# Kernel tuning notes

Hardware: AMD Instinct MI355X
Metric: run time of the kernel (lower is better)

The kernel has to match this reference:

```python
import jax, jax.numpy as jnp
import numpy as np
import math

N, IN_DIM, Z, H, OUT, K = 16384, 64, 128, 1, 3, 16


def setup_inputs() -> dict:
    key = jax.random.key(0)
    ks = jax.random.split(key, 16)

    def lin(k, din, dout):
        kw, kb = jax.random.split(k)
        W = jax.random.normal(kw, (din, dout), jnp.float32) / math.sqrt(din)
        b = jax.random.normal(kb, (dout,), jnp.float32) * 0.01
        return W, b

    x = jax.random.normal(ks[0], (N, IN_DIM), jnp.float32)
    t = jnp.zeros((1,), jnp.float32)
    # layer dims: (in, heads*out) per TransformerConv
    dims = [(IN_DIM, Z * H), (Z * H, (Z // H) * H), (Z * H, (OUT // H) * H)]
    params = {}
    i = 1
    for li, (din, dout) in enumerate(dims, 1):
        for nm in ("q", "k", "v", "s"):
            W, b = lin(ks[i], din, dout)
            i += 1
            params[f"W{nm}{li}"] = W
            params[f"b{nm}{li}"] = b
    return {"t": t, "x": x, **params}


def knn_edge_index(coo, k):
    # kNN graph on 3-D coords (loop=False): edges neighbor(src) -> center(dst)
    n = coo.shape[0]
    sq = jnp.sum(coo * coo, axis=-1)
    d = sq[:, None] + sq[None, :] - 2.0 * (coo @ coo.T)  # [N, N] sq. distances
    d = d.at[jnp.arange(n), jnp.arange(n)].set(jnp.inf)  # exclude self-loops
    _, idx = jax.lax.top_k(-d, k)  # [N, K] nearest neighbor indices
    src = idx.reshape(-1)
    dst = jnp.repeat(jnp.arange(n), k)
    return src, dst


def tconv(x, src, dst, Wq, bq, Wk, bk, Wv, bv, Ws, bs, heads):
    # PyG TransformerConv (concat=True, root_weight=True, no edge_attr)
    n = x.shape[0]
    dout = Wq.shape[1]
    c = dout // heads
    q = (x @ Wq + bq).reshape(n, heads, c)
    kk = (x @ Wk + bk).reshape(n, heads, c)
    v = (x @ Wv + bv).reshape(n, heads, c)
    alpha = jnp.sum(q[dst] * kk[src], axis=-1) / math.sqrt(c)  # [E, H]
    amax = jax.ops.segment_max(alpha, dst, num_segments=n)
    ex = jnp.exp(alpha - amax[dst])
    denom = jax.ops.segment_sum(ex, dst, num_segments=n)
    w = ex / denom[dst]  # softmax over incoming edges per node
    msg = w[:, :, None] * v[src]  # [E, H, C]
    out = jax.ops.segment_sum(msg, dst, num_segments=n).reshape(n, dout)
    return out + x @ Ws + bs  # root/skip connection


def reference(t, x,
              Wq1, bq1, Wk1, bk1, Wv1, bv1, Ws1, bs1,
              Wq2, bq2, Wk2, bk2, Wv2, bv2, Ws2, bs2,
              Wq3, bq3, Wk3, bk3, Wv3, bv3, Ws3, bs3):
    src, dst = knn_edge_index(x[:, :3], K)  # built under no_grad in original
    h = jnp.tanh(tconv(x, src, dst, Wq1, bq1, Wk1, bk1, Wv1, bv1, Ws1, bs1, H))
    h = jnp.tanh(tconv(h, src, dst, Wq2, bq2, Wk2, bk2, Wv2, bv2, Ws2, bs2, H) + h)
    drift_coo = tconv(h, src, dst, Wq3, bq3, Wk3, bk3, Wv3, bv3, Ws3, bs3, H)
    return drift_coo
```

## Files before the change

kernel.cpp:

```cpp
#include <hip/hip_runtime.h>
#include <math.h>

#define NN 16384
#define QPW 2
#define CAP 128
#define WM 64
#define KTOP 17

typedef unsigned long long u64;

__global__ __launch_bounds__(256) void pack_coords(const float* __restrict__ x,
                                                   float4* __restrict__ coo) {
  int i = blockIdx.x * 256 + threadIdx.x;
  float a = x[i * 64 + 0];
  float b = x[i * 64 + 1];
  float c = x[i * 64 + 2];
  coo[i] = make_float4(a, b, c, a * a + b * b + c * c);
}

__device__ __forceinline__ int mbcnt64(u64 mask) {
  return __builtin_amdgcn_mbcnt_hi(
      (unsigned)(mask >> 32),
      __builtin_amdgcn_mbcnt_lo((unsigned)mask, 0));
}

__device__ __forceinline__ unsigned fmap(float d) {
  unsigned ub = __float_as_uint(d);
  return ub ^ ((unsigned)((int)ub >> 31) | 0x80000000u);
}

__device__ __forceinline__ float unfmap(unsigned ub) {
  unsigned fb = (ub & 0x80000000u) ? (ub ^ 0x80000000u) : ~ub;
  return __uint_as_float(fb);
}

__device__ __forceinline__ unsigned short f2bf(float f) {
  unsigned u = __float_as_uint(f);
  return (unsigned short)((u + 0x7FFFu + ((u >> 16) & 1u)) >> 16);
}
__device__ __forceinline__ float bf2f(unsigned short h) {
  return __uint_as_float(((unsigned)h) << 16);
}

__device__ __forceinline__ u64 u64min(u64 a, u64 b) { return a < b ? a : b; }
__device__ __forceinline__ u64 u64max(u64 a, u64 b) { return a > b ? a : b; }

__device__ __forceinline__ void sort128(u64& r0, u64& r1, int lane) {
#pragma unroll
  for (int k = 2; k <= 128; k <<= 1) {
    if (k == 128) {
      u64 lo = u64min(r0, r1);
      r1 = u64max(r0, r1);
      r0 = lo;
    }
#pragma unroll
    for (int jj = (k == 128 ? 32 : (k >> 1)); jj >= 1; jj >>= 1) {
      const bool up = (lane & jj) == 0;
      const bool asc0 = (lane & k) == 0;
      const bool asc1 = ((lane | 64) & k) == 0;
      u64 o0 = __shfl_xor(r0, jj);
      u64 o1 = __shfl_xor(r1, jj);
      r0 = (up == asc0) ? u64min(r0, o0) : u64max(r0, o0);
      r1 = (up == asc1) ? u64min(r1, o1) : u64max(r1, o1);
    }
  }
}

__device__ __forceinline__ void radix_shrink(u64* buf, int& cnt, float& th,
                                             int lane) {
  const u64 k0 = (lane < cnt) ? buf[lane] : ~0ull;
  const u64 k1 = (lane + 64 < cnt) ? buf[lane + 64] : ~0ull;
  const unsigned d0 = (unsigned)(k0 >> 32);
  const unsigned d1 = (unsigned)(k1 >> 32);
  unsigned p = 0u;
#pragma unroll
  for (int b = 31; b >= 0; --b) {
    const unsigned c = p | (1u << b);
    const u64 b0 = __ballot(d0 < c);
    const u64 b1 = __ballot(d1 < c);
    const int n = __popcll(b0) + __popcll(b1);
    if (n < KTOP) p = c;
  }
  const bool v0 = d0 <= p;
  const bool v1 = d1 <= p;
  const u64 m0 = __ballot(v0);
  const u64 m1 = __ballot(v1);
  const int base = __popcll(m0);
  if (v0) buf[mbcnt64(m0)] = k0;
  if (v1) buf[base + mbcnt64(m1)] = k1;
  cnt = base + __popcll(m1);
  th = unfmap(p);
}

__global__ __launch_bounds__(256) void knn_kernel(const float4* __restrict__ coo,
                                                  int* __restrict__ src) {
  __shared__ u64 bufs[4][QPW][CAP];
  const int lane = threadIdx.x & 63;
  const int wid = threadIdx.x >> 6;
  const int node0 = blockIdx.x * (4 * QPW) + wid * QPW;

  float nx[QPW], ny[QPW], nz[QPW], sq[QPW], th[QPW];
  int cnt[QPW];
#pragma unroll
  for (int q = 0; q < QPW; ++q) {
    const float4 me = coo[node0 + q];
    nx[q] = -2.0f * me.x;
    ny[q] = -2.0f * me.y;
    nz[q] = -2.0f * me.z;
    sq[q] = me.w;
    cnt[q] = 0;
  }

  {
    const float4 pa = coo[lane];
    const float4 pb = coo[64 + lane];
#pragma unroll
    for (int q = 0; q < QPW; ++q) {
      const float d0 = sq[q] + fmaf(nx[q], pa.x,
                           fmaf(ny[q], pa.y, fmaf(nz[q], pa.z, pa.w)));
      const float d1 = sq[q] + fmaf(nx[q], pb.x,
                           fmaf(ny[q], pb.y, fmaf(nz[q], pb.z, pb.w)));
      bufs[wid][q][lane] = ((u64)fmap(d0) << 32) | (unsigned)lane;
      bufs[wid][q][64 + lane] = ((u64)fmap(d1) << 32) | (unsigned)(64 + lane);
      cnt[q] = 128;
      radix_shrink(bufs[wid][q], cnt[q], th[q], lane);
    }
  }

  float4 s0 = coo[2 * 64 + lane];
  float4 s1 = coo[3 * 64 + lane];
  float4 s2 = coo[4 * 64 + lane];
  float4 s3 = coo[5 * 64 + lane];

  auto body = [&](const float4 cur, const int step) {
    const int j = step * 64 + lane;
    float dd[QPW];
#pragma unroll
    for (int q = 0; q < QPW; ++q)
      dd[q] = sq[q] + fmaf(nx[q], cur.x,
                           fmaf(ny[q], cur.y, fmaf(nz[q], cur.z, cur.w)));
    u64 mk[QPW];
#pragma unroll
    for (int q = 0; q < QPW; ++q) mk[q] = __ballot(dd[q] <= th[q]);
    if (mk[0] | mk[1]) {
#pragma unroll
      for (int q = 0; q < QPW; ++q) {
        if (mk[q]) {
          if (dd[q] <= th[q])
            bufs[wid][q][cnt[q] + mbcnt64(mk[q])] =
                ((u64)fmap(dd[q]) << 32) | (unsigned)j;
          cnt[q] += __popcll(mk[q]);
          if (cnt[q] >= WM) radix_shrink(bufs[wid][q], cnt[q], th[q], lane);
        }
      }
    }
  };

#pragma unroll 1
  for (int g = 0; g < 63; ++g) {
    const int base = 2 + g * 4;
    body(s0, base + 0);
    s0 = coo[(base + 4) * 64 + lane];
    body(s1, base + 1);
    s1 = coo[(base + 5) * 64 + lane];
    body(s2, base + 2);
    s2 = coo[(base + 6) * 64 + lane];
    body(s3, base + 3);
    s3 = coo[(base + 7) * 64 + lane];
  }
  body(s0, 254);
  body(s1, 255);

#pragma unroll 1
  for (int q = 0; q < QPW; ++q) {
    u64 r0 = (lane < cnt[q]) ? bufs[wid][q][lane] : ~0ull;
    u64 r1 = (lane + 64 < cnt[q]) ? bufs[wid][q][lane + 64] : ~0ull;
    sort128(r0, r1, lane);
    const int idx = (int)(r0 & 0xFFFFFFFFull);
    const u64 selfm = __ballot((lane < KTOP) && (idx == node0 + q));
    const int s = selfm ? (__ffsll((long long)selfm) - 1) : 99;
    const int outrank = lane - (lane > s ? 1 : 0);
    if (lane < KTOP && lane != s && outrank < 16)
      src[(node0 + q) * 16 + outrank] = idx;
  }
}

template <int KD>
__global__ __launch_bounds__(256) void gemm_qkvs(
    const float* __restrict__ X, const float* __restrict__ W0,
    const float* __restrict__ W1, const float* __restrict__ W2,
    const float* __restrict__ W3, const float* __restrict__ B0,
    const float* __restrict__ B1, const float* __restrict__ B2,
    const float* __restrict__ B3, float* __restrict__ qs,
    unsigned short* __restrict__ kvh) {
  __shared__ float As[64][68];
  __shared__ float Bs[64][64];
  const int brow = blockIdx.x * 64;
  const int by = blockIdx.y;
  const int wi = by >> 1;
  const float* W = wi == 0 ? W0 : wi == 1 ? W1 : wi == 2 ? W2 : W3;
  const float* bias = wi == 0 ? B0 : wi == 1 ? B1 : wi == 2 ? B2 : B3;
  const int cbase = (by & 1) * 64;
  const int tx = threadIdx.x & 15;
  const int ty = threadIdx.x >> 4;

  float acc[4][4] = {};
  for (int k0 = 0; k0 < KD; k0 += 64) {
    __syncthreads();
#pragma unroll
    for (int i = 0; i < 4; ++i) {
      const int flat = threadIdx.x * 4 + i * 1024;
      const int r = flat >> 6, kk = flat & 63;
      const float4 v = *(const float4*)&X[(brow + r) * KD + k0 + kk];
      As[kk + 0][r] = v.x;
      As[kk + 1][r] = v.y;
      As[kk + 2][r] = v.z;
      As[kk + 3][r] = v.w;
    }
#pragma unroll
    for (int i = 0; i < 4; ++i) {
      const int flat = threadIdx.x * 4 + i * 1024;
      const int kk = flat >> 6, c = flat & 63;
      *(float4*)&Bs[kk][c] = *(const float4*)&W[(k0 + kk) * 128 + cbase + c];
    }
    __syncthreads();
#pragma unroll 8
    for (int k = 0; k < 64; ++k) {
      const float4 a = *(const float4*)&As[k][ty * 4];
      const float4 b = *(const float4*)&Bs[k][tx * 4];
      const float av[4] = {a.x, a.y, a.z, a.w};
      const float bv[4] = {b.x, b.y, b.z, b.w};
#pragma unroll
      for (int i = 0; i < 4; ++i)
#pragma unroll
        for (int jj = 0; jj < 4; ++jj)
          acc[i][jj] = fmaf(av[i], bv[jj], acc[i][jj]);
    }
  }
  const float4 bi = *(const float4*)&bias[cbase + tx * 4];
  const int col = cbase + tx * 4;
#pragma unroll
  for (int i = 0; i < 4; ++i) {
    const int row = brow + ty * 4 + i;
    float4 o;
    o.x = acc[i][0] + bi.x;
    o.y = acc[i][1] + bi.y;
    o.z = acc[i][2] + bi.z;
    o.w = acc[i][3] + bi.w;
    if (wi == 0) {
      *(float4*)&qs[row * 256 + col] = o;
    } else if (wi == 3) {
      *(float4*)&qs[row * 256 + 128 + col] = o;
    } else {
      ushort4 h;
      h.x = f2bf(o.x);
      h.y = f2bf(o.y);
      h.z = f2bf(o.z);
      h.w = f2bf(o.w);
      *(ushort4*)&kvh[row * 256 + (wi == 1 ? col : 128 + col)] = h;
    }
  }
}

__global__ __launch_bounds__(256) void attn_c128(
    const float* __restrict__ qs, const unsigned short* __restrict__ kvh,
    const int* __restrict__ src, const float* __restrict__ res,
    float* __restrict__ hout, int do_res) {
  const int g = threadIdx.x >> 5;
  const int node = blockIdx.x * 8 + g;
  const int c = threadIdx.x & 31;
  const float4 q4 = ((const float4*)(qs + node * 256))[c];

  int nb[16];
#pragma unroll
  for (int r = 0; r < 16; ++r) nb[r] = src[node * 16 + r];

  float p[16];
#pragma unroll
  for (int r = 0; r < 16; ++r) {
    const ushort4 k4 = ((const ushort4*)(kvh + nb[r] * 256))[c];
    p[r] = q4.x * bf2f(k4.x) + q4.y * bf2f(k4.y) + q4.z * bf2f(k4.z) +
           q4.w * bf2f(k4.w);
  }
#pragma unroll
  for (int o = 16; o; o >>= 1) {
#pragma unroll
    for (int r = 0; r < 16; ++r) p[r] += __shfl_xor(p[r], o);
  }

  float m = p[0];
#pragma unroll
  for (int r = 1; r < 16; ++r) m = fmaxf(m, p[r]);
  float w[16];
  float den = 0.0f;
#pragma unroll
  for (int r = 0; r < 16; ++r) {
    w[r] = __expf((p[r] - m) * 0.088388347648318447f);
    den += w[r];
  }
  const float inv = 1.0f / den;
  float o0 = 0.0f, o1 = 0.0f, o2 = 0.0f, o3 = 0.0f;
#pragma unroll
  for (int r = 0; r < 16; ++r) {
    const ushort4 v4 = ((const ushort4*)(kvh + nb[r] * 256 + 128))[c];
    const float ww = w[r] * inv;
    o0 = fmaf(ww, bf2f(v4.x), o0);
    o1 = fmaf(ww, bf2f(v4.y), o1);
    o2 = fmaf(ww, bf2f(v4.z), o2);
    o3 = fmaf(ww, bf2f(v4.w), o3);
  }
  const float4 s4 = ((const float4*)(qs + node * 256 + 128))[c];
  float r0 = o0 + s4.x, r1 = o1 + s4.y, r2 = o2 + s4.z, r3 = o3 + s4.w;
  if (do_res) {
    const float4 h4 = ((const float4*)(res + node * 128))[c];
    r0 += h4.x;
    r1 += h4.y;
    r2 += h4.z;
    r3 += h4.w;
  }
  ((float4*)(hout + node * 128))[c] =
      make_float4(tanhf(r0), tanhf(r1), tanhf(r2), tanhf(r3));
}

__global__ __launch_bounds__(256) void gemm_qkvs3(
    const float* __restrict__ H, const float* __restrict__ W0,
    const float* __restrict__ W1, const float* __restrict__ W2,
    const float* __restrict__ W3, const float* __restrict__ B0,
    const float* __restrict__ B1, const float* __restrict__ B2,
    const float* __restrict__ B3, float* __restrict__ out) {
  __shared__ float hs[64][132];
  __shared__ float wsh[128 * 12];
  __shared__ float bsh[12];
  const int brow = blockIdx.x * 64;
  if (threadIdx.x < 12) {
    const int mi = threadIdx.x / 3, c = threadIdx.x % 3;
    const float* Bsel = mi == 0 ? B0 : mi == 1 ? B1 : mi == 2 ? B2 : B3;
    bsh[threadIdx.x] = Bsel[c];
  }
  for (int t = threadIdx.x; t < 1536; t += 256) {
    const int k = t / 12, cc = t % 12;
    const int mi = cc / 3, c = cc % 3;
    const float* Wsel = mi == 0 ? W0 : mi == 1 ? W1 : mi == 2 ? W2 : W3;
    wsh[t] = Wsel[k * 3 + c];
  }
#pragma unroll
  for (int i = 0; i < 8; ++i) {
    const int flat = threadIdx.x * 4 + i * 1024;
    const int r = flat >> 7, kk = flat & 127;
    *(float4*)&hs[r][kk] = *(const float4*)&H[(brow + r) * 128 + kk];
  }
  __syncthreads();
  const int r = threadIdx.x >> 2;
  const int part = threadIdx.x & 3;
  float a0 = 0.0f, a1 = 0.0f, a2 = 0.0f;
#pragma unroll 4
  for (int k = 0; k < 128; ++k) {
    const float h = hs[r][k];
    a0 = fmaf(h, wsh[k * 12 + part * 3 + 0], a0);
    a1 = fmaf(h, wsh[k * 12 + part * 3 + 1], a1);
    a2 = fmaf(h, wsh[k * 12 + part * 3 + 2], a2);
  }
  const int row = brow + r;
  out[row * 12 + part * 3 + 0] = a0 + bsh[part * 3 + 0];
  out[row * 12 + part * 3 + 1] = a1 + bsh[part * 3 + 1];
  out[row * 12 + part * 3 + 2] = a2 + bsh[part * 3 + 2];
}

__global__ __launch_bounds__(256) void attn_c3(const float* __restrict__ q3,
                                               const int* __restrict__ src,
                                               float* __restrict__ out) {
  const int gid = blockIdx.x * 256 + threadIdx.x;
  const int node = gid >> 4, r = gid & 15;
  const int j = src[node * 16 + r];
  const float* qn = q3 + node * 12;
  const float* kj = q3 + j * 12 + 3;
  float alpha = (qn[0] * kj[0] + qn[1] * kj[1] + qn[2] * kj[2]) *
                0.57735026918962576f;
  float m = alpha;
#pragma unroll
  for (int o = 8; o; o >>= 1) m = fmaxf(m, __shfl_xor(m, o, 16));
  const float e = __expf(alpha - m);
  float den = e;
#pragma unroll
  for (int o = 8; o; o >>= 1) den += __shfl_xor(den, o, 16);
  const float wgt = e / den;
  const float* vj = q3 + j * 12 + 6;
  float o0 = wgt * vj[0], o1 = wgt * vj[1], o2 = wgt * vj[2];
#pragma unroll
  for (int o = 8; o; o >>= 1) {
    o0 += __shfl_xor(o0, o, 16);
    o1 += __shfl_xor(o1, o, 16);
    o2 += __shfl_xor(o2, o, 16);
  }
  if (r == 0) {
    const float* sn = q3 + node * 12 + 9;
    out[node * 3 + 0] = o0 + sn[0];
    out[node * 3 + 1] = o1 + sn[1];
    out[node * 3 + 2] = o2 + sn[2];
  }
}

extern "C" void kernel_launch(void* const* d_in, const int* in_sizes, int n_in,
                              void* d_out, int out_size, void* d_ws,
                              size_t ws_size, hipStream_t stream) {
  const float* x = (const float*)d_in[1];
  const float* Wq1 = (const float*)d_in[2];
  const float* bq1 = (const float*)d_in[3];
  const float* Wk1 = (const float*)d_in[4];
  const float* bk1 = (const float*)d_in[5];
  const float* Wv1 = (const float*)d_in[6];
  const float* bv1 = (const float*)d_in[7];
  const float* Ws1 = (const float*)d_in[8];
  const float* bs1 = (const float*)d_in[9];
  const float* Wq2 = (const float*)d_in[10];
  const float* bq2 = (const float*)d_in[11];
  const float* Wk2 = (const float*)d_in[12];
  const float* bk2 = (const float*)d_in[13];
  const float* Wv2 = (const float*)d_in[14];
  const float* bv2 = (const float*)d_in[15];
  const float* Ws2 = (const float*)d_in[16];
  const float* bs2 = (const float*)d_in[17];
  const float* Wq3 = (const float*)d_in[18];
  const float* bq3 = (const float*)d_in[19];
  const float* Wk3 = (const float*)d_in[20];
  const float* bk3 = (const float*)d_in[21];
  const float* Wv3 = (const float*)d_in[22];
  const float* bv3 = (const float*)d_in[23];
  const float* Ws3 = (const float*)d_in[24];
  const float* bs3 = (const float*)d_in[25];

  const size_t MB = 1024 * 1024;
  char* ws = (char*)d_ws;
  float* qs = (float*)(ws);
  unsigned short* kvh = (unsigned short*)(ws + 16 * MB);
  float* h1 = (float*)(ws + 24 * MB);
  float* h2 = (float*)(ws + 32 * MB);
  int* src = (int*)(ws + 40 * MB);
  float4* coo = (float4*)(ws + 41 * MB);
  float* q3 = (float*)(ws + 42 * MB);
  float* out = (float*)d_out;

  pack_coords<<<NN / 256, 256, 0, stream>>>(x, coo);
  knn_kernel<<<NN / (4 * QPW), 256, 0, stream>>>(coo, src);
  gemm_qkvs<64><<<dim3(NN / 64, 8), 256, 0, stream>>>(
      x, Wq1, Wk1, Wv1, Ws1, bq1, bk1, bv1, bs1, qs, kvh);
  attn_c128<<<NN / 8, 256, 0, stream>>>(qs, kvh, src, nullptr, h1, 0);
  gemm_qkvs<128><<<dim3(NN / 64, 8), 256, 0, stream>>>(
      h1, Wq2, Wk2, Wv2, Ws2, bq2, bk2, bv2, bs2, qs, kvh);
  attn_c128<<<NN / 8, 256, 0, stream>>>(qs, kvh, src, h1, h2, 1);
  gemm_qkvs3<<<NN / 64, 256, 0, stream>>>(h2, Wq3, Wk3, Wv3, Ws3, bq3, bk3,
                                          bv3, bs3, q3);
  attn_c3<<<NN * 16 / 256, 256, 0, stream>>>(q3, src, out);
}
```

Before: 306.1 us.

## Replace brute-force kNN with uniform-grid spatial search

Replaces the O(N^2) brute-force kNN scan with a uniform 32^3 grid. A count/scan/scatter pass bins points into cells, then each wavefront searches outward shell by shell and stops once the current 17th-best distance is within the distance to the shell boundary. This removes the full scan over all 16384 candidates per query that dominated the runtime, at the cost of several small extra launches and atomics. Within-cell scatter order is set by atomics, so the order of candidates with equal distances can differ from before.

```diff
diff --git a/kernel.cpp b/kernel.cpp
--- a/kernel.cpp
+++ b/kernel.cpp
@@ -6,6 +6,10 @@
 #define CAP 128
 #define WM 64
 #define KTOP 17
+#define G 32
+#define GLO (-6.0f)
+#define GW (12.0f / G)
+#define GINVW (G / 12.0f)
 
 typedef unsigned long long u64;
 
@@ -92,97 +96,152 @@
   th = unfmap(p);
 }
 
-__global__ __launch_bounds__(256) void knn_kernel(const float4* __restrict__ coo,
-                                                  int* __restrict__ src) {
-  __shared__ u64 bufs[4][QPW][CAP];
+__device__ __forceinline__ int cell_of(float v) {
+  int c = (int)floorf((v - GLO) * GINVW);
+  return min(max(c, 0), G - 1);
+}
+
+__global__ __launch_bounds__(256) void grid_zero(int* __restrict__ counts) {
+  counts[blockIdx.x * 256 + threadIdx.x] = 0;
+}
+
+__global__ __launch_bounds__(256) void grid_count(const float4* __restrict__ coo,
+                                                  int* __restrict__ counts) {
+  const int i = blockIdx.x * 256 + threadIdx.x;
+  const float4 p = coo[i];
+  const int cell = (cell_of(p.z) * G + cell_of(p.y)) * G + cell_of(p.x);
+  atomicAdd(&counts[cell], 1);
+}
+
+__global__ __launch_bounds__(1024) void grid_scan(const int* __restrict__ counts,
+                                                  int* __restrict__ cellStart,
+                                                  int* __restrict__ cursor) {
+  __shared__ int part[1024];
+  const int t = threadIdx.x;
+  const int base = t * (G * G * G / 1024);
+  int sum = 0;
+  for (int i = 0; i < G * G * G / 1024; ++i) sum += counts[base + i];
+  part[t] = sum;
+  __syncthreads();
+  for (int off = 1; off < 1024; off <<= 1) {
+    int v = (t >= off) ? part[t - off] : 0;
+    __syncthreads();
+    part[t] += v;
+    __syncthreads();
+  }
+  int run = (t == 0) ? 0 : part[t - 1];
+  for (int i = 0; i < G * G * G / 1024; ++i) {
+    const int c = counts[base + i];
+    cellStart[base + i] = run;
+    cursor[base + i] = run;
+    run += c;
+  }
+  if (t == 1023) cellStart[G * G * G] = run;
+}
+
+__global__ __launch_bounds__(256) void grid_scatter(
+    const float4* __restrict__ coo, int* __restrict__ cursor,
+    float4* __restrict__ scoo, int* __restrict__ sidx) {
+  const int i = blockIdx.x * 256 + threadIdx.x;
+  const float4 p = coo[i];
+  const int cell = (cell_of(p.z) * G + cell_of(p.y)) * G + cell_of(p.x);
+  const int pos = atomicAdd(&cursor[cell], 1);
+  scoo[pos] = p;
+  sidx[pos] = i;
+}
+
+__global__ __launch_bounds__(256) void knn_grid(
+    const float4* __restrict__ scoo, const int* __restrict__ sidx,
+    const int* __restrict__ cellStart, const float4* __restrict__ coo,
+    int* __restrict__ src) {
+  __shared__ u64 bufs[4][CAP];
   const int lane = threadIdx.x & 63;
   const int wid = threadIdx.x >> 6;
-  const int node0 = blockIdx.x * (4 * QPW) + wid * QPW;
-
-  float nx[QPW], ny[QPW], nz[QPW], sq[QPW], th[QPW];
-  int cnt[QPW];
-#pragma unroll
-  for (int q = 0; q < QPW; ++q) {
-    const float4 me = coo[node0 + q];
-    nx[q] = -2.0f * me.x;
-    ny[q] = -2.0f * me.y;
-    nz[q] = -2.0f * me.z;
-    sq[q] = me.w;
-    cnt[q] = 0;
-  }
-
-  {
-    const float4 pa = coo[lane];
-    const float4 pb = coo[64 + lane];
-#pragma unroll
-    for (int q = 0; q < QPW; ++q) {
-      const float d0 = sq[q] + fmaf(nx[q], pa.x,
-                           fmaf(ny[q], pa.y, fmaf(nz[q], pa.z, pa.w)));
-      const float d1 = sq[q] + fmaf(nx[q], pb.x,
-                           fmaf(ny[q], pb.y, fmaf(nz[q], pb.z, pb.w)));
-      bufs[wid][q][lane] = ((u64)fmap(d0) << 32) | (unsigned)lane;
-      bufs[wid][q][64 + lane] = ((u64)fmap(d1) << 32) | (unsigned)(64 + lane);
-      cnt[q] = 128;
-      radix_shrink(bufs[wid][q], cnt[q], th[q], lane);
-    }
-  }
-
-  float4 s0 = coo[2 * 64 + lane];
-  float4 s1 = coo[3 * 64 + lane];
-  float4 s2 = coo[4 * 64 + lane];
-  float4 s3 = coo[5 * 64 + lane];
-
-  auto body = [&](const float4 cur, const int step) {
-    const int j = step * 64 + lane;
-    float dd[QPW];
-#pragma unroll
-    for (int q = 0; q < QPW; ++q)
-      dd[q] = sq[q] + fmaf(nx[q], cur.x,
-                           fmaf(ny[q], cur.y, fmaf(nz[q], cur.z, cur.w)));
-    u64 mk[QPW];
-#pragma unroll
-    for (int q = 0; q < QPW; ++q) mk[q] = __ballot(dd[q] <= th[q]);
-    if (mk[0] | mk[1]) {
-#pragma unroll
-      for (int q = 0; q < QPW; ++q) {
-        if (mk[q]) {
-          if (dd[q] <= th[q])
-            bufs[wid][q][cnt[q] + mbcnt64(mk[q])] =
-                ((u64)fmap(dd[q]) << 32) | (unsigned)j;
-          cnt[q] += __popcll(mk[q]);
-          if (cnt[q] >= WM) radix_shrink(bufs[wid][q], cnt[q], th[q], lane);
+  const int node = blockIdx.x * 4 + wid;
+  u64* buf = bufs[wid];
+
+  const float4 me = coo[node];
+  const float nx = -2.0f * me.x, ny = -2.0f * me.y, nz = -2.0f * me.z;
+  const float sq = me.w;
+  const int hx = cell_of(me.x), hy = cell_of(me.y), hz = cell_of(me.z);
+
+  float th = __builtin_inff();
+  int cnt = 0;
+
+  auto runrange = [&](int x0, int x1, int y, int z) {
+    const int b = (z * G + y) * G;
+    const int rs = cellStart[b + x0];
+    const int re = cellStart[b + x1 + 1];
+    for (int bs = rs; bs < re; bs += 64) {
+      const int i = bs + lane;
+      const int ic = min(i, NN - 1);
+      const float4 p = scoo[ic];
+      const int id = sidx[ic];
+      float acc = fmaf(nz, p.z, p.w);
+      acc = fmaf(ny, p.y, acc);
+      acc = fmaf(nx, p.x, acc);
+      const float d = sq + acc;
+      const bool val = (i < re) && (d <= th);
+      const u64 mk = __ballot(val);
+      if (mk) {
+        if (val)
+          buf[cnt + mbcnt64(mk)] = ((u64)fmap(d) << 32) | (unsigned)id;
+        cnt += __popcll(mk);
+        if (cnt >= WM) radix_shrink(buf, cnt, th, lane);
+      }
+    }
+  };
+
+  for (int dz = -1; dz <= 1; ++dz) {
+    const int z = hz + dz;
+    if (z < 0 || z >= G) continue;
+    for (int dy = -1; dy <= 1; ++dy) {
+      const int y = hy + dy;
+      if (y < 0 || y >= G) continue;
+      runrange(max(hx - 1, 0), min(hx + 1, G - 1), y, z);
+    }
+  }
+
+  int s = 1;
+  while (true) {
+    if (cnt >= KTOP) {
+      radix_shrink(buf, cnt, th, lane);
+      float dmin = 1e30f;
+      if (hx - s > 0) dmin = fminf(dmin, me.x - (GLO + (hx - s) * GW));
+      if (hx + s < G - 1) dmin = fminf(dmin, (GLO + (hx + s + 1) * GW) - me.x);
+      if (hy - s > 0) dmin = fminf(dmin, me.y - (GLO + (hy - s) * GW));
+      if (hy + s < G - 1) dmin = fminf(dmin, (GLO + (hy + s + 1) * GW) - me.y);
+      if (hz - s > 0) dmin = fminf(dmin, me.z - (GLO + (hz - s) * GW));
+      if (hz + s < G - 1) dmin = fminf(dmin, (GLO + (hz + s + 1) * GW) - me.z);
+      dmin = fmaxf(dmin, 0.0f);
+      if (th <= dmin * dmin * 0.9999f) break;
+    }
+    ++s;
+    if (s > G) break;
+    for (int dz = -s; dz <= s; ++dz) {
+      const int z = hz + dz;
+      if (z < 0 || z >= G) continue;
+      for (int dy = -s; dy <= s; ++dy) {
+        const int y = hy + dy;
+        if (y < 0 || y >= G) continue;
+        if (dz == -s || dz == s || dy == -s || dy == s) {
+          runrange(max(hx - s, 0), min(hx + s, G - 1), y, z);
+        } else {
+          if (hx - s >= 0) runrange(hx - s, hx - s, y, z);
+          if (hx + s <= G - 1) runrange(hx + s, hx + s, y, z);
         }
       }
     }
-  };
-
-#pragma unroll 1
-  for (int g = 0; g < 63; ++g) {
-    const int base = 2 + g * 4;
-    body(s0, base + 0);
-    s0 = coo[(base + 4) * 64 + lane];
-    body(s1, base + 1);
-    s1 = coo[(base + 5) * 64 + lane];
-    body(s2, base + 2);
-    s2 = coo[(base + 6) * 64 + lane];
-    body(s3, base + 3);
-    s3 = coo[(base + 7) * 64 + lane];
-  }
-  body(s0, 254);
-  body(s1, 255);
-
-#pragma unroll 1
-  for (int q = 0; q < QPW; ++q) {
-    u64 r0 = (lane < cnt[q]) ? bufs[wid][q][lane] : ~0ull;
-    u64 r1 = (lane + 64 < cnt[q]) ? bufs[wid][q][lane + 64] : ~0ull;
-    sort128(r0, r1, lane);
-    const int idx = (int)(r0 & 0xFFFFFFFFull);
-    const u64 selfm = __ballot((lane < KTOP) && (idx == node0 + q));
-    const int s = selfm ? (__ffsll((long long)selfm) - 1) : 99;
-    const int outrank = lane - (lane > s ? 1 : 0);
-    if (lane < KTOP && lane != s && outrank < 16)
-      src[(node0 + q) * 16 + outrank] = idx;
-  }
+  }
+
+  u64 r0 = (lane < cnt) ? buf[lane] : ~0ull;
+  u64 r1 = (lane + 64 < cnt) ? buf[lane + 64] : ~0ull;
+  sort128(r0, r1, lane);
+  const int idx = (int)(r0 & 0xFFFFFFFFull);
+  const u64 selfm = __ballot((lane < KTOP) && (idx == node));
+  const int sf = selfm ? (__ffsll((long long)selfm) - 1) : 99;
+  const int outrank = lane - (lane > sf ? 1 : 0);
+  if (lane < KTOP && lane != sf && outrank < 16) src[node * 16 + outrank] = idx;
 }
 
 template <int KD>
@@ -438,10 +497,19 @@
   int* src = (int*)(ws + 40 * MB);
   float4* coo = (float4*)(ws + 41 * MB);
   float* q3 = (float*)(ws + 42 * MB);
+  int* counts = (int*)(ws + 43 * MB);
+  int* cursor = (int*)(ws + 43 * MB + 128 * 1024);
+  int* cellStart = (int*)(ws + 43 * MB + 256 * 1024);
+  float4* scoo = (float4*)(ws + 44 * MB);
+  int* sidx = (int*)(ws + 44 * MB + 256 * 1024);
   float* out = (float*)d_out;
 
   pack_coords<<<NN / 256, 256, 0, stream>>>(x, coo);
-  knn_kernel<<<NN / (4 * QPW), 256, 0, stream>>>(coo, src);
+  grid_zero<<<G * G * G / 256, 256, 0, stream>>>(counts);
+  grid_count<<<NN / 256, 256, 0, stream>>>(coo, counts);
+  grid_scan<<<1, 1024, 0, stream>>>(counts, cellStart, cursor);
+  grid_scatter<<<NN / 256, 256, 0, stream>>>(coo, cursor, scoo, sidx);
+  knn_grid<<<NN / 4, 256, 0, stream>>>(scoo, sidx, cellStart, coo, src);
   gemm_qkvs<64><<<dim3(NN / 64, 8), 256, 0, stream>>>(
       x, Wq1, Wk1, Wv1, Ws1, bq1, bk1, bv1, bs1, qs, kvh);
   attn_c128<<<NN / 8, 256, 0, stream>>>(qs, kvh, src, nullptr, h1, 0);
```

Result: slower. 366.7 us (+19.8%).
